# Kernel tuning notes

Measured on AMD Instinct MI355X. Metric: run time of the kernel, lower is better.

## Reference

```python
import jax, jax.numpy as jnp
import numpy as np

# Directable[TL_table[i]] for i = 0..7: (dx, dy) with dx=horizontal shift, dy=vertical shift
# dx=+1 -> shift right (zero-fill col 0), dx=-1 -> shift left; dy=+1 -> shift down, dy=-1 -> shift up.
DIRS = [(1, 1), (0, 1), (-1, 1), (1, 0), (-1, 0), (1, -1), (0, -1), (-1, -1)]


def _shift(img, dx, dy):
    # img: [B, H, W]; zero-padded shift equivalent to bmm with the sparse translation matrices
    if dx == 1:
        img = jnp.pad(img[..., :-1], ((0, 0), (0, 0), (1, 0)))
    elif dx == -1:
        img = jnp.pad(img[..., 1:], ((0, 0), (0, 0), (0, 1)))
    if dy == 1:
        img = jnp.pad(img[:, :-1, :], ((0, 0), (1, 0), (0, 0)))
    elif dy == -1:
        img = jnp.pad(img[:, 1:, :], ((0, 0), (0, 1), (0, 0)))
    return img


def _bce(p, t):
    # torch F.binary_cross_entropy clamps log terms at -100
    logp = jnp.maximum(jnp.log(p), -100.0)
    log1mp = jnp.maximum(jnp.log(1.0 - p), -100.0)
    return -jnp.mean(t * logp + (1.0 - t) * log1mp)


def setup_inputs() -> dict:
    key = jax.random.key(0)
    k1, k2, k3 = jax.random.split(key, 3)
    B, C, H, W = 16, 8, 512, 512
    c_map = jax.random.normal(k1, (B, C, H, W), dtype=jnp.float32)
    target = jax.random.randint(k2, (B, 1, H, W), 0, 2, dtype=jnp.int32)
    con_target = jax.random.randint(k3, (B, C, H, W), 0, 2, dtype=jnp.int32)
    return {"c_map": c_map, "target": target, "con_target": con_target}


def reference(c_map, target, con_target):
    target = target.astype(jnp.float32)        # [B,1,H,W]
    con_target = con_target.astype(jnp.float32)  # [B,8,H,W]

    p = jax.nn.sigmoid(c_map)  # [B,8,H,W]

    # Bilateral voting: shifted[i] = shift(p[:, 7-i]) in direction DIRS[i]
    shifted = jnp.stack(
        [_shift(p[:, 7 - i], dx, dy) for i, (dx, dy) in enumerate(DIRS)], axis=1
    )  # [B,8,H,W]
    vote_out = p * shifted                       # [B,8,H,W] (== bimap.squeeze(1))
    final_pred = jnp.max(vote_out, axis=1, keepdims=True)  # [B,1,H,W]

    # dice loss (sums over dims (1,2) of the 4D tensors, as in the original)
    smooth = 0.001
    i_sum = jnp.sum(target, axis=(1, 2))
    j_sum = jnp.sum(final_pred, axis=(1, 2))
    inter = jnp.sum(target * final_pred, axis=(1, 2))
    loss_dice = jnp.mean(1.0 - (2.0 * inter + smooth) / (i_sum + j_sum + smooth))

    # edge (decouple) loss
    sum_conn = jnp.sum(con_target, axis=1)  # [B,H,W]
    edge = ((sum_conn < 8) & (sum_conn > 0)).astype(p.dtype)
    pred_min = jnp.min(vote_out, axis=1) * edge
    decouple_loss = _bce(pred_min, jnp.zeros_like(pred_min))

    bce_loss = _bce(final_pred, target)
    conmap_l = _bce(p, con_target)
    bimap_l = _bce(vote_out, con_target)

    return 0.8 * conmap_l + decouple_loss + 0.2 * bimap_l + bce_loss + loss_dice
```

## Files before the change

kernel.cpp:

```cpp
#include <hip/hip_runtime.h>

namespace {
constexpr int Bn = 16, Cn = 8, Hn = 512, Wn = 512;
constexpr int HW  = Hn * Wn;
constexpr int CHW = Cn * HW;
constexpr int NCOL = Bn * Wn;
constexpr int GX   = Hn / 4;
constexpr int NBLK = GX * Bn;
constexpr int FBLK = 32;

__device__ __forceinline__ float frcp(float x) { return __builtin_amdgcn_rcpf(x); }
}


__global__ __launch_bounds__(256, 4) void bicon_main(
    const float* __restrict__ c_map,
    const int*   __restrict__ target,
    const int*   __restrict__ con_target,
    float* __restrict__ col_i, float* __restrict__ col_j, float* __restrict__ col_x,
    double* __restrict__ bscal)
{
    const int tx = threadIdx.x;
    const int ty = threadIdx.y;
    const int b  = blockIdx.y;
    const int h  = blockIdx.x * 4 + ty;
    const int wq = tx << 3;
    const int base = h * Wn + wq;

    const float* cm = c_map      + (size_t)b * CHW;
    const int*   ct = con_target + (size_t)b * CHW;
    const int*   tg = target     + (size_t)b * HW;

    unsigned lo = 0u, hi = 0u;
#pragma unroll
    for (int c = 0; c < 8; ++c) {
        const int4 u0 = *(const int4*)(ct + c * HW + base);
        const int4 u1 = *(const int4*)(ct + c * HW + base + 4);
        lo |= ((unsigned)u0.x << c) | ((unsigned)u0.y << (8 + c)) |
              ((unsigned)u0.z << (16 + c)) | ((unsigned)u0.w << (24 + c));
        hi |= ((unsigned)u1.x << c) | ((unsigned)u1.y << (8 + c)) |
              ((unsigned)u1.z << (16 + c)) | ((unsigned)u1.w << (24 + c));
    }
    auto bit = [&](int k, int c) -> int {
        return (int)(((k < 4 ? lo >> (8 * k + c) : hi >> (8 * (k - 4) + c))) & 1u);
    };

    float s_con = 0.f, s_bi = 0.f, s_bce = 0.f, s_dec = 0.f;
    float vmax[8], vmin[8];
#pragma unroll
    for (int k = 0; k < 8; ++k) { vmax[k] = 0.f; vmin[k] = 2.f; }

    auto center = [&](int c, float s[8]) {
        const float* p = cm + c * HW + base;
        const float4 v0 = *(const float4*)p;
        const float4 v1 = *(const float4*)(p + 4);
        const float xs[8] = {v0.x, v0.y, v0.z, v0.w, v1.x, v1.y, v1.z, v1.w};
#pragma unroll
        for (int k = 0; k < 8; ++k) {
            const float e = __expf(-xs[k]);
            const float d = 1.f + e;
            s[k] = frcp(d);
            const float logd = __logf(d);
            s_con += fmaxf(bit(k, c) ? -logd : (-xs[k] - logd), -100.f);
        }
    };
    auto nbrrow = [&](int c, int dy, float sp[8]) {
        const int hn = h + dy;
        if ((unsigned)hn < (unsigned)Hn) {
            const float* p = cm + c * HW + hn * Wn + wq;
            const float4 v0 = *(const float4*)p;
            const float4 v1 = *(const float4*)(p + 4);
            const float xs[8] = {v0.x, v0.y, v0.z, v0.w, v1.x, v1.y, v1.z, v1.w};
#pragma unroll
            for (int k = 0; k < 8; ++k) sp[k] = frcp(1.f + __expf(-xs[k]));
        } else {
#pragma unroll
            for (int k = 0; k < 8; ++k) sp[k] = 0.f;
        }
    };
    auto shplus = [&](const float sp[8], float n[8]) {
#pragma unroll
        for (int k = 0; k < 7; ++k) n[k] = sp[k + 1];
        const float t = __shfl_down(sp[0], 1);
        n[7] = (tx == 63) ? 0.f : t;
    };
    auto shminus = [&](const float sp[8], float n[8]) {
#pragma unroll
        for (int k = 7; k > 0; --k) n[k] = sp[k - 1];
        const float t = __shfl_up(sp[7], 1);
        n[0] = (tx == 0) ? 0.f : t;
    };
    auto vote = [&](int i, const float si[8], const float nn[8]) {
#pragma unroll
        for (int k = 0; k < 8; ++k) {
            const float v = si[k] * nn[k];
            vmax[k] = fmaxf(vmax[k], v);
            vmin[k] = fminf(vmin[k], v);
            s_bi += fmaxf(__logf(bit(k, i) ? v : 1.f - v), -100.f);
        }
    };

    {
        float sa[8], sb[8], sp[8], n[8];
        center(0, sa); center(7, sb);
        nbrrow(0, +1, sp); shplus(sp, n);  vote(7, sb, n);
        nbrrow(7, -1, sp); shminus(sp, n); vote(0, sa, n);
    }
    {
        float sa[8], sb[8], sp[8];
        center(1, sa); center(6, sb);
        nbrrow(1, +1, sp); vote(6, sb, sp);
        nbrrow(6, -1, sp); vote(1, sa, sp);
    }
    {
        float sa[8], sb[8], sp[8], n[8];
        center(2, sa); center(5, sb);
        nbrrow(2, +1, sp); shminus(sp, n); vote(5, sb, n);
        nbrrow(5, -1, sp); shplus(sp, n);  vote(2, sa, n);
    }
    {
        float sa[8], sb[8], n[8];
        center(3, sa); center(4, sb);
        shplus(sa, n);  vote(4, sb, n);
        shminus(sb, n); vote(3, sa, n);
    }

    const int4 t0 = *(const int4*)(tg + base);
    const int4 t1 = *(const int4*)(tg + base + 4);
    const int tk[8] = {t0.x, t0.y, t0.z, t0.w, t1.x, t1.y, t1.z, t1.w};

    __shared__ float cred[3][4][512];
#pragma unroll
    for (int k = 0; k < 8; ++k) {
        const float fm = vmax[k];
        s_bce += fmaxf(__logf(tk[k] ? fm : 1.f - fm), -100.f);
        const int sc = __popc((int)((k < 4 ? lo >> (8 * k) : hi >> (8 * (k - 4))) & 0xffu));
        const float le = fmaxf(__logf(1.f - vmin[k]), -100.f);
        s_dec += (sc > 0 && sc < 8) ? le : 0.f;
        cred[0][ty][wq + k] = (float)tk[k];
        cred[1][ty][wq + k] = fm;
        cred[2][ty][wq + k] = tk[k] ? fm : 0.f;
    }

#pragma unroll
    for (int off = 32; off > 0; off >>= 1) {
        s_con += __shfl_down(s_con, off);
        s_bi  += __shfl_down(s_bi,  off);
        s_bce += __shfl_down(s_bce, off);
        s_dec += __shfl_down(s_dec, off);
    }
    __shared__ float wred[4][4];
    if (tx == 0) {
        wred[ty][0] = s_con; wred[ty][1] = s_bi;
        wred[ty][2] = s_bce; wred[ty][3] = s_dec;
    }
    __syncthreads();

    const int tid = ty * 64 + tx;
#pragma unroll
    for (int j = tid; j < 512; j += 256) {
        const float a0 = cred[0][0][j] + cred[0][1][j] + cred[0][2][j] + cred[0][3][j];
        const float a1 = cred[1][0][j] + cred[1][1][j] + cred[1][2][j] + cred[1][3][j];
        const float a2 = cred[2][0][j] + cred[2][1][j] + cred[2][2][j] + cred[2][3][j];
        atomicAdd(&col_i[b * Wn + j], a0);
        atomicAdd(&col_j[b * Wn + j], a1);
        atomicAdd(&col_x[b * Wn + j], a2);
    }
    if (tid < 4) {
        bscal[((size_t)blockIdx.y * GX + blockIdx.x) * 4 + tid] =
            (double)(wred[0][tid] + wred[1][tid] + wred[2][tid] + wred[3][tid]);
    }
}

__global__ __launch_bounds__(256) void bicon_finish(
    const float* __restrict__ col_i,
    const float* __restrict__ col_j,
    const float* __restrict__ col_x,
    const double* __restrict__ bscal,
    float* __restrict__ out)
{
    const int tid = threadIdx.x;
    const int col = blockIdx.x * 256 + tid;

    double part;
    {
        const float fi = col_i[col], fj = col_j[col], fx = col_x[col];
        part = (1.0 - (2.0 * (double)fx + 0.001) /
                      ((double)fi + (double)fj + 0.001)) / 8192.0;
    }
    if (tid < 64) {
        const int s = blockIdx.x * 64 + tid;
        const double c0 = bscal[s * 4 + 0], c1 = bscal[s * 4 + 1];
        const double c2 = bscal[s * 4 + 2], c3 = bscal[s * 4 + 3];
        part += -0.8 * c0 / 33554432.0 - 0.2 * c1 / 33554432.0
                - c2 / 4194304.0 - c3 / 4194304.0;
    }
#pragma unroll
    for (int off = 32; off > 0; off >>= 1) part += __shfl_down(part, off);
    __shared__ double red[4];
    if ((tid & 63) == 0) red[tid >> 6] = part;
    __syncthreads();
    if (tid == 0) atomicAdd(out, (float)(red[0] + red[1] + red[2] + red[3]));
}

extern "C" void kernel_launch(void* const* d_in, const int* in_sizes, int n_in,
                              void* d_out, int out_size, void* d_ws, size_t ws_size,
                              hipStream_t stream) {
    const float* c_map      = (const float*)d_in[0];
    const int*   target     = (const int*)d_in[1];
    const int*   con_target = (const int*)d_in[2];
    float* out = (float*)d_out;

    char* ws = (char*)d_ws;
    float*  col_i = (float*)ws;
    float*  col_j = col_i + NCOL;
    float*  col_x = col_j + NCOL;
    double* bscal = (double*)(ws + 3 * NCOL * sizeof(float));

    hipMemsetAsync(d_ws, 0, 3 * NCOL * sizeof(float), stream);
    hipMemsetAsync(d_out, 0, sizeof(float), stream);

    dim3 grid(GX, Bn);
    dim3 block(64, 4);
    bicon_main<<<grid, block, 0, stream>>>(c_map, target, con_target,
                                           col_i, col_j, col_x, bscal);
    bicon_finish<<<FBLK, 256, 0, stream>>>(col_i, col_j, col_x, bscal, out);
}
```

Baseline: 348.3 us.

## Process 4 pixels per thread over 8 rows, load shifted neighbors unaligned

Each thread now handles 4 pixels instead of 8 and loops over several rows per block, with blocks covering 8 rows. Horizontal neighbours are fetched with unaligned 4-wide loads at offset ±1 instead of cross-lane shuffles, and per-column dice sums are kept in registers across rows, cutting shared-memory traffic and column atomics. This trades lower per-thread register pressure and fewer atomics for extra, partly misaligned global loads and half as many blocks, which may lower parallelism.

```diff
diff --git a/kernel.cpp b/kernel.cpp
--- a/kernel.cpp
+++ b/kernel.cpp
@@ -1,15 +1,18 @@
 #include <hip/hip_runtime.h>
 
 namespace {
-constexpr int Bn = 16, Cn = 8, Hn = 512, Wn = 512;
+constexpr int Bn = 16, Hn = 512, Wn = 512;
 constexpr int HW  = Hn * Wn;
-constexpr int CHW = Cn * HW;
+constexpr int CHW = 8 * HW;
 constexpr int NCOL = Bn * Wn;
-constexpr int GX   = Hn / 4;
+constexpr int ROWS = 8;
+constexpr int GX   = Hn / ROWS;
 constexpr int NBLK = GX * Bn;
 constexpr int FBLK = 32;
 
 __device__ __forceinline__ float frcp(float x) { return __builtin_amdgcn_rcpf(x); }
+
+typedef float f4u __attribute__((ext_vector_type(4), aligned(4)));
 }
 
 
@@ -20,126 +23,122 @@
     float* __restrict__ col_i, float* __restrict__ col_j, float* __restrict__ col_x,
     double* __restrict__ bscal)
 {
-    const int tx = threadIdx.x;
-    const int ty = threadIdx.y;
-    const int b  = blockIdx.y;
-    const int h  = blockIdx.x * 4 + ty;
-    const int wq = tx << 3;
-    const int base = h * Wn + wq;
+    const int tid  = threadIdx.x;
+    const int lane = tid & 63;
+    const int wv   = tid >> 6;
+    const int half = wv & 1;
+    const int rofs = wv >> 1;
+    const int b    = blockIdx.y;
+    const int h0   = blockIdx.x * ROWS;
+    const int wq   = half * 256 + lane * 4;
 
     const float* cm = c_map      + (size_t)b * CHW;
     const int*   ct = con_target + (size_t)b * CHW;
     const int*   tg = target     + (size_t)b * HW;
 
-    unsigned lo = 0u, hi = 0u;
-#pragma unroll
-    for (int c = 0; c < 8; ++c) {
-        const int4 u0 = *(const int4*)(ct + c * HW + base);
-        const int4 u1 = *(const int4*)(ct + c * HW + base + 4);
-        lo |= ((unsigned)u0.x << c) | ((unsigned)u0.y << (8 + c)) |
-              ((unsigned)u0.z << (16 + c)) | ((unsigned)u0.w << (24 + c));
-        hi |= ((unsigned)u1.x << c) | ((unsigned)u1.y << (8 + c)) |
-              ((unsigned)u1.z << (16 + c)) | ((unsigned)u1.w << (24 + c));
-    }
-    auto bit = [&](int k, int c) -> int {
-        return (int)(((k < 4 ? lo >> (8 * k + c) : hi >> (8 * (k - 4) + c))) & 1u);
-    };
-
     float s_con = 0.f, s_bi = 0.f, s_bce = 0.f, s_dec = 0.f;
-    float vmax[8], vmin[8];
-#pragma unroll
-    for (int k = 0; k < 8; ++k) { vmax[k] = 0.f; vmin[k] = 2.f; }
-
-    auto center = [&](int c, float s[8]) {
-        const float* p = cm + c * HW + base;
-        const float4 v0 = *(const float4*)p;
-        const float4 v1 = *(const float4*)(p + 4);
-        const float xs[8] = {v0.x, v0.y, v0.z, v0.w, v1.x, v1.y, v1.z, v1.w};
-#pragma unroll
-        for (int k = 0; k < 8; ++k) {
-            const float e = __expf(-xs[k]);
-            const float d = 1.f + e;
-            s[k] = frcp(d);
-            const float logd = __logf(d);
-            s_con += fmaxf(bit(k, c) ? -logd : (-xs[k] - logd), -100.f);
-        }
-    };
-    auto nbrrow = [&](int c, int dy, float sp[8]) {
-        const int hn = h + dy;
-        if ((unsigned)hn < (unsigned)Hn) {
-            const float* p = cm + c * HW + hn * Wn + wq;
-            const float4 v0 = *(const float4*)p;
-            const float4 v1 = *(const float4*)(p + 4);
-            const float xs[8] = {v0.x, v0.y, v0.z, v0.w, v1.x, v1.y, v1.z, v1.w};
-#pragma unroll
-            for (int k = 0; k < 8; ++k) sp[k] = frcp(1.f + __expf(-xs[k]));
-        } else {
-#pragma unroll
-            for (int k = 0; k < 8; ++k) sp[k] = 0.f;
-        }
-    };
-    auto shplus = [&](const float sp[8], float n[8]) {
-#pragma unroll
-        for (int k = 0; k < 7; ++k) n[k] = sp[k + 1];
-        const float t = __shfl_down(sp[0], 1);
-        n[7] = (tx == 63) ? 0.f : t;
-    };
-    auto shminus = [&](const float sp[8], float n[8]) {
-#pragma unroll
-        for (int k = 7; k > 0; --k) n[k] = sp[k - 1];
-        const float t = __shfl_up(sp[7], 1);
-        n[0] = (tx == 0) ? 0.f : t;
-    };
-    auto vote = [&](int i, const float si[8], const float nn[8]) {
-#pragma unroll
-        for (int k = 0; k < 8; ++k) {
-            const float v = si[k] * nn[k];
-            vmax[k] = fmaxf(vmax[k], v);
-            vmin[k] = fminf(vmin[k], v);
-            s_bi += fmaxf(__logf(bit(k, i) ? v : 1.f - v), -100.f);
-        }
-    };
-
-    {
-        float sa[8], sb[8], sp[8], n[8];
-        center(0, sa); center(7, sb);
-        nbrrow(0, +1, sp); shplus(sp, n);  vote(7, sb, n);
-        nbrrow(7, -1, sp); shminus(sp, n); vote(0, sa, n);
-    }
-    {
-        float sa[8], sb[8], sp[8];
-        center(1, sa); center(6, sb);
-        nbrrow(1, +1, sp); vote(6, sb, sp);
-        nbrrow(6, -1, sp); vote(1, sa, sp);
-    }
-    {
-        float sa[8], sb[8], sp[8], n[8];
-        center(2, sa); center(5, sb);
-        nbrrow(2, +1, sp); shminus(sp, n); vote(5, sb, n);
-        nbrrow(5, -1, sp); shplus(sp, n);  vote(2, sa, n);
-    }
-    {
-        float sa[8], sb[8], n[8];
-        center(3, sa); center(4, sb);
-        shplus(sa, n);  vote(4, sb, n);
-        shminus(sb, n); vote(3, sa, n);
-    }
-
-    const int4 t0 = *(const int4*)(tg + base);
-    const int4 t1 = *(const int4*)(tg + base + 4);
-    const int tk[8] = {t0.x, t0.y, t0.z, t0.w, t1.x, t1.y, t1.z, t1.w};
-
-    __shared__ float cred[3][4][512];
-#pragma unroll
-    for (int k = 0; k < 8; ++k) {
-        const float fm = vmax[k];
-        s_bce += fmaxf(__logf(tk[k] ? fm : 1.f - fm), -100.f);
-        const int sc = __popc((int)((k < 4 ? lo >> (8 * k) : hi >> (8 * (k - 4))) & 0xffu));
-        const float le = fmaxf(__logf(1.f - vmin[k]), -100.f);
-        s_dec += (sc > 0 && sc < 8) ? le : 0.f;
-        cred[0][ty][wq + k] = (float)tk[k];
-        cred[1][ty][wq + k] = fm;
-        cred[2][ty][wq + k] = tk[k] ? fm : 0.f;
+    float ci[4] = {0, 0, 0, 0}, cj[4] = {0, 0, 0, 0}, cx[4] = {0, 0, 0, 0};
+
+#pragma unroll 1
+    for (int r = 0; r < ROWS / 2; ++r) {
+        const int h    = h0 + 2 * r + rofs;
+        const int base = h * Wn + wq;
+
+        unsigned lo = 0u;
+#pragma unroll
+        for (int c = 0; c < 8; ++c) {
+            const int4 u = *(const int4*)(ct + c * HW + base);
+            lo |= ((unsigned)u.x << c)        | ((unsigned)u.y << (8 + c)) |
+                  ((unsigned)u.z << (16 + c)) | ((unsigned)u.w << (24 + c));
+        }
+
+        float vmax[4], vmin[4];
+#pragma unroll
+        for (int k = 0; k < 4; ++k) { vmax[k] = 0.f; vmin[k] = 2.f; }
+
+        auto center = [&](int c, float s[4]) {
+            const float4 v = *(const float4*)(cm + c * HW + base);
+            const float xs[4] = {v.x, v.y, v.z, v.w};
+#pragma unroll
+            for (int k = 0; k < 4; ++k) {
+                const float e = __expf(-xs[k]);
+                const float d = 1.f + e;
+                s[k] = frcp(d);
+                const float logd = __logf(d);
+                s_con += fmaxf(((lo >> (8 * k + c)) & 1u) ? -logd : (-xs[k] - logd),
+                               -100.f);
+            }
+        };
+        auto nbr = [&](int c, int dy, int dx, float n[4]) {
+            const int hn = h + dy;
+            if ((unsigned)hn < (unsigned)Hn) {
+                const f4u v = *(const f4u*)(cm + c * HW + hn * Wn + (wq + dx));
+                const float xs[4] = {v.x, v.y, v.z, v.w};
+#pragma unroll
+                for (int k = 0; k < 4; ++k) n[k] = frcp(1.f + __expf(-xs[k]));
+                if (dx == 1 && wq == Wn - 4) n[3] = 0.f;
+                if (dx == -1 && wq == 0)     n[0] = 0.f;
+            } else {
+#pragma unroll
+                for (int k = 0; k < 4; ++k) n[k] = 0.f;
+            }
+        };
+        auto vote = [&](int i, const float si[4], const float nn[4]) {
+#pragma unroll
+            for (int k = 0; k < 4; ++k) {
+                const float v = si[k] * nn[k];
+                vmax[k] = fmaxf(vmax[k], v);
+                vmin[k] = fminf(vmin[k], v);
+                s_bi += fmaxf(__logf(((lo >> (8 * k + i)) & 1u) ? v : 1.f - v),
+                              -100.f);
+            }
+        };
+
+        {
+            float pa[4], pb[4], na[4], nb_[4];
+            center(0, pa); center(7, pb);
+            nbr(0, +1, +1, na);  vote(7, pb, na);
+            nbr(7, -1, -1, nb_); vote(0, pa, nb_);
+        }
+        {
+            float pa[4], pb[4], na[4], nb_[4];
+            center(1, pa); center(6, pb);
+            nbr(1, +1, 0, na);   vote(6, pb, na);
+            nbr(6, -1, 0, nb_);  vote(1, pa, nb_);
+        }
+        {
+            float pa[4], pb[4], na[4], nb_[4];
+            center(2, pa); center(5, pb);
+            nbr(2, +1, -1, na);  vote(5, pb, na);
+            nbr(5, -1, +1, nb_); vote(2, pa, nb_);
+        }
+        {
+            float pa[4], pb[4], na[4], nb_[4];
+            center(3, pa); center(4, pb);
+            nbr(3, 0, +1, na);   vote(4, pb, na);
+            nbr(4, 0, -1, nb_);  vote(3, pa, nb_);
+        }
+
+        const int4 t = *(const int4*)(tg + base);
+        const int tk[4] = {t.x, t.y, t.z, t.w};
+#pragma unroll
+        for (int k = 0; k < 4; ++k) {
+            const float fm = vmax[k];
+            s_bce += fmaxf(__logf(tk[k] ? fm : 1.f - fm), -100.f);
+            const int sc = __popc((int)((lo >> (8 * k)) & 0xffu));
+            s_dec += (sc > 0 && sc < 8) ? fmaxf(__logf(1.f - vmin[k]), -100.f) : 0.f;
+            ci[k] += (float)tk[k];
+            cj[k] += fm;
+            cx[k] += tk[k] ? fm : 0.f;
+        }
+    }
+
+    __shared__ float cred[3][4][256];
+#pragma unroll
+    for (int k = 0; k < 4; ++k) {
+        cred[0][wv][(lane << 2) + k] = ci[k];
+        cred[1][wv][(lane << 2) + k] = cj[k];
+        cred[2][wv][(lane << 2) + k] = cx[k];
     }
 
 #pragma unroll
@@ -150,18 +149,18 @@
         s_dec += __shfl_down(s_dec, off);
     }
     __shared__ float wred[4][4];
-    if (tx == 0) {
-        wred[ty][0] = s_con; wred[ty][1] = s_bi;
-        wred[ty][2] = s_bce; wred[ty][3] = s_dec;
+    if (lane == 0) {
+        wred[wv][0] = s_con; wred[wv][1] = s_bi;
+        wred[wv][2] = s_bce; wred[wv][3] = s_dec;
     }
     __syncthreads();
 
-    const int tid = ty * 64 + tx;
 #pragma unroll
     for (int j = tid; j < 512; j += 256) {
-        const float a0 = cred[0][0][j] + cred[0][1][j] + cred[0][2][j] + cred[0][3][j];
-        const float a1 = cred[1][0][j] + cred[1][1][j] + cred[1][2][j] + cred[1][3][j];
-        const float a2 = cred[2][0][j] + cred[2][1][j] + cred[2][2][j] + cred[2][3][j];
+        const int hj = j >> 8, cidx = j & 255;
+        const float a0 = cred[0][hj][cidx] + cred[0][hj + 2][cidx];
+        const float a1 = cred[1][hj][cidx] + cred[1][hj + 2][cidx];
+        const float a2 = cred[2][hj][cidx] + cred[2][hj + 2][cidx];
         atomicAdd(&col_i[b * Wn + j], a0);
         atomicAdd(&col_j[b * Wn + j], a1);
         atomicAdd(&col_x[b * Wn + j], a2);
@@ -188,8 +187,8 @@
         part = (1.0 - (2.0 * (double)fx + 0.001) /
                       ((double)fi + (double)fj + 0.001)) / 8192.0;
     }
-    if (tid < 64) {
-        const int s = blockIdx.x * 64 + tid;
+    if (tid < 32) {
+        const int s = blockIdx.x * 32 + tid;
         const double c0 = bscal[s * 4 + 0], c1 = bscal[s * 4 + 1];
         const double c2 = bscal[s * 4 + 2], c3 = bscal[s * 4 + 3];
         part += -0.8 * c0 / 33554432.0 - 0.2 * c1 / 33554432.0
@@ -221,7 +220,7 @@
     hipMemsetAsync(d_out, 0, sizeof(float), stream);
 
     dim3 grid(GX, Bn);
-    dim3 block(64, 4);
+    dim3 block(256);
     bicon_main<<<grid, block, 0, stream>>>(c_map, target, con_target,
                                            col_i, col_j, col_x, bscal);
     bicon_finish<<<FBLK, 256, 0, stream>>>(col_i, col_j, col_x, bscal, out);
```

Result: no change. 352.0 us (+1.0%).
